# Performance work log

Hardware: AMD Instinct MI355X
Metric: run time of the kernel (lower is better)

## Reference

```python
import jax, jax.numpy as jnp
import numpy as np

N = 262144          # ray samples
L = 16              # grid levels
T = 2 ** 19         # hash table entries per level
F = 2               # features per entry
NMIN, NMAX = 16, 2048
SB = 1.0            # scene_bound
DW, CW = 64, 64     # density / color MLP widths

_PRIMES = jnp.array([1, 2654435761, 805459861], dtype=jnp.uint32)
_OFFS = jnp.asarray(np.stack(np.meshgrid([0, 1], [0, 1], [0, 1], indexing='ij'), -1).reshape(8, 3), dtype=jnp.uint32)  # 8 cube corners


def _scalings():
    g = np.exp((np.log(NMAX) - np.log(NMIN)) / (L - 1))
    return jnp.asarray(np.floor(NMIN * g ** np.arange(L)), dtype=jnp.float32)  # (L,)


def hash_encode(pos01, table):
    # pos01: (N,3) in [0,1]; table: (L*T, F)
    scaled = pos01[:, None, :] * _scalings()[None, :, None]        # (N,L,3)
    floor = jnp.floor(scaled)
    frac = scaled - floor                                          # (N,L,3)
    corners = floor.astype(jnp.uint32)[:, :, None, :] + _OFFS[None, None]  # (N,L,8,3)
    h = corners * _PRIMES                                          # uint32 wraparound hashing
    idx = (h[..., 0] ^ h[..., 1] ^ h[..., 2]) % jnp.uint32(T)      # (N,L,8)
    idx = idx.astype(jnp.int32) + (jnp.arange(L, dtype=jnp.int32) * T)[None, :, None]
    feats = table[idx]                                             # (N,L,8,F) gather
    sel = _OFFS.astype(bool)[None, None]                           # (1,1,8,3)
    w = jnp.prod(jnp.where(sel, frac[:, :, None, :], 1.0 - frac[:, :, None, :]), axis=-1)  # (N,L,8)
    out = jnp.einsum('nlcf,nlc->nlf', feats, w)                    # trilinear interp
    return out.reshape(out.shape[0], L * F)                        # (N, 32)


def sh_encode(d):
    # 4th-order real spherical harmonics, 16 components (instant-ngp convention)
    x, y, z = d[..., 0], d[..., 1], d[..., 2]
    xx, yy, zz = x * x, y * y, z * z
    xy, yz, xz = x * y, y * z, x * z
    return jnp.stack([
        jnp.full_like(x, 0.28209479177387814),
        -0.48860251190291987 * y,
        0.48860251190291987 * z,
        -0.48860251190291987 * x,
        1.0925484305920792 * xy,
        -1.0925484305920792 * yz,
        0.94617469575755997 * zz - 0.31539156525252005,
        -1.0925484305920792 * xz,
        0.54627421529603959 * (xx - yy),
        0.59004358992664352 * y * (-3.0 * xx + yy),
        2.8906114426405538 * xy * z,
        0.45704579946446572 * y * (1.0 - 5.0 * zz),
        0.3731763325901154 * z * (5.0 * zz - 3.0),
        0.45704579946446572 * x * (1.0 - 5.0 * zz),
        1.445305721320277 * z * (xx - yy),
        0.59004358992664352 * x * (xx - 3.0 * yy),
    ], axis=-1)  # (N,16)


def setup_inputs() -> dict:
    key = jax.random.key(0)
    ks = jax.random.split(key, 10)
    position = jax.random.uniform(ks[0], (N, 3), jnp.float32, -SB, SB)
    d = jax.random.normal(ks[1], (N, 3), jnp.float32)
    direction = d / jnp.linalg.norm(d, axis=-1, keepdims=True)
    hash_table = jax.random.uniform(ks[2], (L * T, F), jnp.float32, -1e-4, 1e-4)
    def dense(k, fin, fout, std):
        return (jax.random.normal(k, (fin, fout), jnp.float32) * std,
                jnp.zeros((fout,), jnp.float32))
    w1, b1 = dense(ks[3], L * F, DW, 0.01)      # normal() init in source
    w2, b2 = dense(ks[4], DW, 16, 0.01)
    w3, b3 = dense(ks[5], 16 + 16, CW, 0.01)
    w4, b4 = dense(ks[6], CW, CW, 0.01)
    w5, b5 = dense(ks[7], CW, 3, 0.1)           # default lecun-ish scale
    return dict(position=position, direction=direction, hash_table=hash_table,
                w1=w1, b1=b1, w2=w2, b2=b2, w3=w3, b3=b3, w4=w4, b4=b4, w5=w5, b5=b5)


def reference(position, direction, hash_table, w1, b1, w2, b2, w3, b3, w4, b4, w5, b5):
    p = (position + SB) / (2.0 * SB)                 # -> [0,1]
    enc = hash_encode(p, hash_table)                 # (N,32)
    h = jax.nn.relu(enc @ w1 + b1)                   # density MLP
    h = h @ w2 + b2                                  # (N,16)
    density = jnp.exp(h[:, 0:1])                     # exponential_density_activation
    sh = sh_encode(direction)                        # (N,16)
    c = jnp.concatenate([h, sh], axis=-1)            # (N,32)
    c = jax.nn.relu(c @ w3 + b3)
    c = jax.nn.relu(c @ w4 + b4)
    c = c @ w5 + b5
    color = jax.nn.sigmoid(c)                        # high_dynamic_range=False
    return jnp.concatenate([density, color], axis=-1)  # (N,4) drgbs
```

## Files before the change

kernel.cpp:

```cpp
#include <hip/hip_runtime.h>
#include <cmath>

namespace {
constexpr int kN = 262144;
constexpr int kL = 16;
constexpr int kT = 1 << 19;
constexpr unsigned kTMask = kT - 1;

typedef __attribute__((ext_vector_type(8))) short short8;
typedef __attribute__((ext_vector_type(4))) float f32x4;
typedef __attribute__((ext_vector_type(4))) unsigned short ushort4v;

struct Scales { float s[kL]; };

__device__ __forceinline__ unsigned short f2bf(float f) {
    unsigned u = __builtin_bit_cast(unsigned, f);
    return (unsigned short)((u + 0x7FFFu + ((u >> 16) & 1u)) >> 16);
}

__global__ __launch_bounds__(256) void prep_w(
    const float* __restrict__ w1, const float* __restrict__ w2,
    const float* __restrict__ w3, const float* __restrict__ w4,
    const float* __restrict__ w5, unsigned short* __restrict__ out)
{
    const int i = blockIdx.x * 256 + threadIdx.x;
    const int f = i >> 9;
    const int l = (i >> 3) & 63;
    const int e = i & 7;
    const int cl = l & 15;
    const int kg = l >> 4;
    float v = 0.0f;
    if (f < 4) {
        v = w1[(kg * 8 + e) * 64 + f * 16 + cl];
    } else if (f < 6) {
        const int q = f - 4;
        v = w2[(q * 32 + kg * 8 + e) * 16 + cl];
    } else if (f < 10) {
        v = w3[(kg * 8 + e) * 64 + (f - 6) * 16 + cl];
    } else if (f < 18) {
        const int g = f - 10, q = g >> 2, nt = g & 3;
        v = w4[(q * 32 + kg * 8 + e) * 64 + nt * 16 + cl];
    } else {
        const int q = f - 18;
        v = (cl < 3) ? w5[(q * 32 + kg * 8 + e) * 3 + cl] : 0.0f;
    }
    out[i] = f2bf(v);
}

__global__ __launch_bounds__(256) void ngp_encode(
    const float* __restrict__ pos,
    const float2* __restrict__ table,
    unsigned* __restrict__ enc,
    Scales sc)
{
    const int bid = blockIdx.x;
    const int l = bid >> 10;
    const int n = ((bid & 1023) << 8) | threadIdx.x;

    const float s = sc.s[l];
    const float2* __restrict__ tl = table + (size_t)l * kT;

    const float px = (pos[n * 3 + 0] + 1.0f) * 0.5f;
    const float py = (pos[n * 3 + 1] + 1.0f) * 0.5f;
    const float pz = (pos[n * 3 + 2] + 1.0f) * 0.5f;
    const float sx = px * s, sy = py * s, sz = pz * s;
    const float fx = floorf(sx), fy = floorf(sy), fz = floorf(sz);
    const float rx = sx - fx, ry = sy - fy, rz = sz - fz;
    const unsigned cx = (unsigned)fx, cy = (unsigned)fy, cz = (unsigned)fz;

    const unsigned hy0 = cy * 2654435761u, hy1 = (cy + 1u) * 2654435761u;
    const unsigned hz0 = cz * 805459861u,  hz1 = (cz + 1u) * 805459861u;

    float4 pr[4];
    float2 ex[4];
    unsigned idx0v[4], hyzv[4];

    #pragma unroll
    for (int j = 0; j < 4; ++j) {
        const unsigned hyz = ((j >> 1) ? hy1 : hy0) ^ ((j & 1) ? hz1 : hz0);
        hyzv[j] = hyz;
        const unsigned idx0 = (cx ^ hyz) & kTMask;
        idx0v[j] = idx0;
        pr[j] = *reinterpret_cast<const float4*>(tl + (idx0 & ~1u));
    }

    if (cx & 1u) {
        const unsigned cx1 = cx + 1u;
        #pragma unroll
        for (int j = 0; j < 4; ++j)
            ex[j] = tl[(cx1 ^ hyzv[j]) & kTMask];
    }

    const bool odd = (cx & 1u) != 0u;
    const float wx0 = 1.0f - rx, wx1 = rx;
    float f0 = 0.f, f1 = 0.f;
    #pragma unroll
    for (int j = 0; j < 4; ++j) {
        const float wyz = ((j >> 1) ? ry : 1.0f - ry) *
                          ((j & 1) ? rz : 1.0f - rz);
        const bool hi = (idx0v[j] & 1u) != 0u;
        const float c0x = hi ? pr[j].z : pr[j].x;
        const float c0y = hi ? pr[j].w : pr[j].y;
        const float c1x = odd ? ex[j].x : (hi ? pr[j].x : pr[j].z);
        const float c1y = odd ? ex[j].y : (hi ? pr[j].y : pr[j].w);
        f0 = fmaf(c0x, wx0 * wyz, f0);
        f1 = fmaf(c0y, wx0 * wyz, f1);
        f0 = fmaf(c1x, wx1 * wyz, f0);
        f1 = fmaf(c1y, wx1 * wyz, f1);
    }
    enc[(size_t)l * kN + n] = (unsigned)f2bf(f0) | ((unsigned)f2bf(f1) << 16);
}

__global__ __launch_bounds__(256) void ngp_mlp_mfma(
    const unsigned* __restrict__ enc,
    const unsigned short* __restrict__ wbf,
    const float* __restrict__ dir,
    const float* __restrict__ b1, const float* __restrict__ b2,
    const float* __restrict__ b3, const float* __restrict__ b4,
    const float* __restrict__ b5,
    float* __restrict__ out)
{
    __shared__ unsigned short sA[4][4096];
    __shared__ unsigned short sB[4][2048];

    const int tid = threadIdx.x;
    const int wid = tid >> 6;
    const int l   = tid & 63;
    const int cl  = l & 15;
    const int kg  = l >> 4;
    unsigned short* __restrict__ A_ = sA[wid];
    unsigned short* __restrict__ B_ = sB[wid];
    const int gbase = blockIdx.x * 256 + wid * 64;

    {
        const int s = gbase + l;
        const float x = dir[s * 3 + 0], y = dir[s * 3 + 1], z = dir[s * 3 + 2];
        const float xx = x * x, yy = y * y, zz = z * z;
        const float xy = x * y, yz = y * z, xz = x * z;
        float sh[16];
        sh[0] = 0.28209479177387814f;
        sh[1] = -0.48860251190291987f * y;
        sh[2] = 0.48860251190291987f * z;
        sh[3] = -0.48860251190291987f * x;
        sh[4] = 1.0925484305920792f * xy;
        sh[5] = -1.0925484305920792f * yz;
        sh[6] = 0.94617469575755997f * zz - 0.31539156525252005f;
        sh[7] = -1.0925484305920792f * xz;
        sh[8] = 0.54627421529603959f * (xx - yy);
        sh[9] = 0.59004358992664352f * y * (-3.0f * xx + yy);
        sh[10] = 2.8906114426405538f * xy * z;
        sh[11] = 0.45704579946446572f * y * (1.0f - 5.0f * zz);
        sh[12] = 0.3731763325901154f * z * (5.0f * zz - 3.0f);
        sh[13] = 0.45704579946446572f * x * (1.0f - 5.0f * zz);
        sh[14] = 1.445305721320277f * z * (xx - yy);
        sh[15] = 0.59004358992664352f * x * (xx - 3.0f * yy);
        #pragma unroll
        for (int j = 0; j < 16; ++j)
            B_[(l >> 4) * 512 + (16 + j) * 16 + (l & 15)] = f2bf(sh[j]);
    }

    short8 A1[4];
    #pragma unroll
    for (int m = 0; m < 4; ++m) {
        #pragma unroll
        for (int j = 0; j < 4; ++j) {
            const unsigned v = enc[(size_t)(kg * 4 + j) * kN + (gbase + m * 16 + cl)];
            A1[m][2 * j]     = (short)(v & 0xFFFFu);
            A1[m][2 * j + 1] = (short)(v >> 16);
        }
    }
    {
        short8 B1[4];
        #pragma unroll
        for (int nt = 0; nt < 4; ++nt)
            B1[nt] = *reinterpret_cast<const short8*>(&wbf[(size_t)(nt) * 512 + l * 8]);

        f32x4 acc[4][4];
        #pragma unroll
        for (int nt = 0; nt < 4; ++nt) {
            const float bv = b1[nt * 16 + cl];
            #pragma unroll
            for (int m = 0; m < 4; ++m) {
                acc[m][nt][0] = bv; acc[m][nt][1] = bv; acc[m][nt][2] = bv; acc[m][nt][3] = bv;
            }
        }
        #pragma unroll
        for (int m = 0; m < 4; ++m)
            #pragma unroll
            for (int nt = 0; nt < 4; ++nt)
                acc[m][nt] = __builtin_amdgcn_mfma_f32_16x16x32_bf16(A1[m], B1[nt], acc[m][nt], 0, 0, 0);

        #pragma unroll
        for (int m = 0; m < 4; ++m) {
            #pragma unroll
            for (int nt = 0; nt < 4; ++nt) {
                ushort4v pk;
                #pragma unroll
                for (int r = 0; r < 4; ++r) pk[r] = f2bf(fmaxf(acc[m][nt][r], 0.0f));
                *reinterpret_cast<ushort4v*>(&A_[m * 1024 + (nt * 16 + cl) * 16 + kg * 4]) = pk;
            }
        }
    }

    {
        short8 A2[4][2];
        #pragma unroll
        for (int m = 0; m < 4; ++m)
            #pragma unroll
            for (int q = 0; q < 2; ++q)
                #pragma unroll
                for (int e = 0; e < 8; ++e)
                    A2[m][q][e] = (short)A_[m * 1024 + (q * 32 + kg * 8 + e) * 16 + cl];

        short8 B2[2];
        #pragma unroll
        for (int q = 0; q < 2; ++q)
            B2[q] = *reinterpret_cast<const short8*>(&wbf[(size_t)(4 + q) * 512 + l * 8]);

        f32x4 acc[4];
        const float bv = b2[cl];
        #pragma unroll
        for (int m = 0; m < 4; ++m) { acc[m][0] = bv; acc[m][1] = bv; acc[m][2] = bv; acc[m][3] = bv; }
        #pragma unroll
        for (int m = 0; m < 4; ++m)
            #pragma unroll
            for (int q = 0; q < 2; ++q)
                acc[m] = __builtin_amdgcn_mfma_f32_16x16x32_bf16(A2[m][q], B2[q], acc[m], 0, 0, 0);

        #pragma unroll
        for (int m = 0; m < 4; ++m) {
            if (cl == 0) {
                #pragma unroll
                for (int r = 0; r < 4; ++r)
                    out[(size_t)(gbase + m * 16 + kg * 4 + r) * 4 + 0] = expf(acc[m][r]);
            }
            ushort4v pk;
            #pragma unroll
            for (int r = 0; r < 4; ++r) pk[r] = f2bf(acc[m][r]);
            *reinterpret_cast<ushort4v*>(&B_[m * 512 + cl * 16 + kg * 4]) = pk;
        }
    }

    {
        short8 A3[4];
        #pragma unroll
        for (int m = 0; m < 4; ++m)
            #pragma unroll
            for (int e = 0; e < 8; ++e)
                A3[m][e] = (short)B_[m * 512 + (kg * 8 + e) * 16 + cl];

        short8 B3[4];
        #pragma unroll
        for (int nt = 0; nt < 4; ++nt)
            B3[nt] = *reinterpret_cast<const short8*>(&wbf[(size_t)(6 + nt) * 512 + l * 8]);

        f32x4 acc[4][4];
        #pragma unroll
        for (int nt = 0; nt < 4; ++nt) {
            const float bv = b3[nt * 16 + cl];
            #pragma unroll
            for (int m = 0; m < 4; ++m) {
                acc[m][nt][0] = bv; acc[m][nt][1] = bv; acc[m][nt][2] = bv; acc[m][nt][3] = bv;
            }
        }
        #pragma unroll
        for (int m = 0; m < 4; ++m)
            #pragma unroll
            for (int nt = 0; nt < 4; ++nt)
                acc[m][nt] = __builtin_amdgcn_mfma_f32_16x16x32_bf16(A3[m], B3[nt], acc[m][nt], 0, 0, 0);

        #pragma unroll
        for (int m = 0; m < 4; ++m) {
            #pragma unroll
            for (int nt = 0; nt < 4; ++nt) {
                ushort4v pk;
                #pragma unroll
                for (int r = 0; r < 4; ++r) pk[r] = f2bf(fmaxf(acc[m][nt][r], 0.0f));
                *reinterpret_cast<ushort4v*>(&A_[m * 1024 + (nt * 16 + cl) * 16 + kg * 4]) = pk;
            }
        }
    }

    {
        short8 A4[4][2];
        #pragma unroll
        for (int m = 0; m < 4; ++m)
            #pragma unroll
            for (int q = 0; q < 2; ++q)
                #pragma unroll
                for (int e = 0; e < 8; ++e)
                    A4[m][q][e] = (short)A_[m * 1024 + (q * 32 + kg * 8 + e) * 16 + cl];

        short8 B4[2][4];
        #pragma unroll
        for (int q = 0; q < 2; ++q)
            #pragma unroll
            for (int nt = 0; nt < 4; ++nt)
                B4[q][nt] = *reinterpret_cast<const short8*>(&wbf[(size_t)(10 + q * 4 + nt) * 512 + l * 8]);

        f32x4 acc[4][4];
        #pragma unroll
        for (int nt = 0; nt < 4; ++nt) {
            const float bv = b4[nt * 16 + cl];
            #pragma unroll
            for (int m = 0; m < 4; ++m) {
                acc[m][nt][0] = bv; acc[m][nt][1] = bv; acc[m][nt][2] = bv; acc[m][nt][3] = bv;
            }
        }
        #pragma unroll
        for (int m = 0; m < 4; ++m)
            #pragma unroll
            for (int nt = 0; nt < 4; ++nt)
                #pragma unroll
                for (int q = 0; q < 2; ++q)
                    acc[m][nt] = __builtin_amdgcn_mfma_f32_16x16x32_bf16(A4[m][q], B4[q][nt], acc[m][nt], 0, 0, 0);

        #pragma unroll
        for (int m = 0; m < 4; ++m) {
            #pragma unroll
            for (int nt = 0; nt < 4; ++nt) {
                ushort4v pk;
                #pragma unroll
                for (int r = 0; r < 4; ++r) pk[r] = f2bf(fmaxf(acc[m][nt][r], 0.0f));
                *reinterpret_cast<ushort4v*>(&A_[m * 1024 + (nt * 16 + cl) * 16 + kg * 4]) = pk;
            }
        }
    }

    {
        short8 A5[4][2];
        #pragma unroll
        for (int m = 0; m < 4; ++m)
            #pragma unroll
            for (int q = 0; q < 2; ++q)
                #pragma unroll
                for (int e = 0; e < 8; ++e)
                    A5[m][q][e] = (short)A_[m * 1024 + (q * 32 + kg * 8 + e) * 16 + cl];

        short8 B5[2];
        #pragma unroll
        for (int q = 0; q < 2; ++q)
            B5[q] = *reinterpret_cast<const short8*>(&wbf[(size_t)(18 + q) * 512 + l * 8]);

        f32x4 acc[4];
        const float bv = (cl < 3) ? b5[cl] : 0.0f;
        #pragma unroll
        for (int m = 0; m < 4; ++m) { acc[m][0] = bv; acc[m][1] = bv; acc[m][2] = bv; acc[m][3] = bv; }
        #pragma unroll
        for (int m = 0; m < 4; ++m)
            #pragma unroll
            for (int q = 0; q < 2; ++q)
                acc[m] = __builtin_amdgcn_mfma_f32_16x16x32_bf16(A5[m][q], B5[q], acc[m], 0, 0, 0);

        if (cl < 3) {
            #pragma unroll
            for (int m = 0; m < 4; ++m)
                #pragma unroll
                for (int r = 0; r < 4; ++r)
                    out[(size_t)(gbase + m * 16 + kg * 4 + r) * 4 + 1 + cl] =
                        1.0f / (1.0f + expf(-acc[m][r]));
        }
    }
}

}

extern "C" void kernel_launch(void* const* d_in, const int* in_sizes, int n_in,
                              void* d_out, int out_size, void* d_ws, size_t ws_size,
                              hipStream_t stream) {
    (void)in_sizes; (void)n_in; (void)out_size; (void)ws_size;

    Scales sc;
    const double g = exp((log(2048.0) - log(16.0)) / 15.0);
    for (int l = 0; l < kL; ++l) sc.s[l] = (float)floor(16.0 * pow(g, (double)l));

    const float*  pos   = (const float*)d_in[0];
    const float*  dir   = (const float*)d_in[1];
    const float2* table = (const float2*)d_in[2];
    const float *w1 = (const float*)d_in[3],  *b1 = (const float*)d_in[4];
    const float *w2 = (const float*)d_in[5],  *b2 = (const float*)d_in[6];
    const float *w3 = (const float*)d_in[7],  *b3 = (const float*)d_in[8];
    const float *w4 = (const float*)d_in[9],  *b4 = (const float*)d_in[10];
    const float *w5 = (const float*)d_in[11], *b5 = (const float*)d_in[12];
    float* out = (float*)d_out;

    unsigned short* wbf = (unsigned short*)d_ws;
    unsigned* enc = (unsigned*)((char*)d_ws + 32768);

    prep_w<<<40, 256, 0, stream>>>(w1, w2, w3, w4, w5, wbf);
    ngp_encode<<<kL * 1024, 256, 0, stream>>>(pos, table, enc, sc);
    ngp_mlp_mfma<<<kN / 256, 256, 0, stream>>>(enc, wbf, dir,
        b1, b2, b3, b4, b5, out);
}
```

Measured before the change: 147.4 us.

## Spatially bucket-sort ray samples before hash encoding to improve gather locality

Adds histogram, scan and scatter kernels that reorder samples by a coarse 16^3 spatial cell, so the encode kernel processes nearby points together and hash-table gathers for coarse levels share cache lines. The MLP reads sorted directions and writes outputs back through a sorted-to-original index map. This costs extra launches, contended atomics, a single-block scan, and scattered output writes.

```diff
diff --git a/kernel.cpp b/kernel.cpp
--- a/kernel.cpp
+++ b/kernel.cpp
@@ -6,6 +6,7 @@
 constexpr int kL = 16;
 constexpr int kT = 1 << 19;
 constexpr unsigned kTMask = kT - 1;
+constexpr int kB = 4096;
 
 typedef __attribute__((ext_vector_type(8))) short short8;
 typedef __attribute__((ext_vector_type(4))) float f32x4;
@@ -47,8 +48,69 @@
     out[i] = f2bf(v);
 }
 
+__global__ __launch_bounds__(256) void bucket_hist(
+    const float* __restrict__ pos,
+    unsigned short* __restrict__ key,
+    unsigned* __restrict__ hist)
+{
+    const int n = blockIdx.x * 256 + threadIdx.x;
+    const float px = (pos[n * 3 + 0] + 1.0f) * 0.5f;
+    const float py = (pos[n * 3 + 1] + 1.0f) * 0.5f;
+    const float pz = (pos[n * 3 + 2] + 1.0f) * 0.5f;
+    const int cx = min(15, (int)(px * 16.0f));
+    const int cy = min(15, (int)(py * 16.0f));
+    const int cz = min(15, (int)(pz * 16.0f));
+    const int k = (cx << 8) | (cy << 4) | cz;
+    key[n] = (unsigned short)k;
+    atomicAdd(&hist[k], 1u);
+}
+
+__global__ __launch_bounds__(1024) void bucket_scan(
+    const unsigned* __restrict__ hist,
+    unsigned* __restrict__ cursor)
+{
+    __shared__ unsigned s[1024];
+    const int t = threadIdx.x;
+    const unsigned v0 = hist[4 * t], v1 = hist[4 * t + 1];
+    const unsigned v2 = hist[4 * t + 2], v3 = hist[4 * t + 3];
+    const unsigned a0 = v0, a1 = a0 + v1, a2 = a1 + v2, a3 = a2 + v3;
+    s[t] = a3;
+    __syncthreads();
+    for (int off = 1; off < 1024; off <<= 1) {
+        unsigned x = 0;
+        if (t >= off) x = s[t - off];
+        __syncthreads();
+        if (t >= off) s[t] += x;
+        __syncthreads();
+    }
+    const unsigned base = (t > 0) ? s[t - 1] : 0u;
+    cursor[4 * t]     = base;
+    cursor[4 * t + 1] = base + a0;
+    cursor[4 * t + 2] = base + a1;
+    cursor[4 * t + 3] = base + a2;
+}
+
+__global__ __launch_bounds__(256) void bucket_scatter(
+    const float* __restrict__ pos, const float* __restrict__ dir,
+    const unsigned short* __restrict__ key,
+    unsigned* __restrict__ cursor,
+    float* __restrict__ spos, float* __restrict__ sdir,
+    unsigned* __restrict__ s2o)
+{
+    const int n = blockIdx.x * 256 + threadIdx.x;
+    const unsigned k = key[n];
+    const unsigned i = atomicAdd(&cursor[k], 1u);
+    s2o[i] = (unsigned)n;
+    spos[i * 3 + 0] = pos[n * 3 + 0];
+    spos[i * 3 + 1] = pos[n * 3 + 1];
+    spos[i * 3 + 2] = pos[n * 3 + 2];
+    sdir[i * 3 + 0] = dir[n * 3 + 0];
+    sdir[i * 3 + 1] = dir[n * 3 + 1];
+    sdir[i * 3 + 2] = dir[n * 3 + 2];
+}
+
 __global__ __launch_bounds__(256) void ngp_encode(
-    const float* __restrict__ pos,
+    const float* __restrict__ spos,
     const float2* __restrict__ table,
     unsigned* __restrict__ enc,
     Scales sc)
@@ -60,9 +122,9 @@
     const float s = sc.s[l];
     const float2* __restrict__ tl = table + (size_t)l * kT;
 
-    const float px = (pos[n * 3 + 0] + 1.0f) * 0.5f;
-    const float py = (pos[n * 3 + 1] + 1.0f) * 0.5f;
-    const float pz = (pos[n * 3 + 2] + 1.0f) * 0.5f;
+    const float px = (spos[n * 3 + 0] + 1.0f) * 0.5f;
+    const float py = (spos[n * 3 + 1] + 1.0f) * 0.5f;
+    const float pz = (spos[n * 3 + 2] + 1.0f) * 0.5f;
     const float sx = px * s, sy = py * s, sz = pz * s;
     const float fx = floorf(sx), fy = floorf(sy), fz = floorf(sz);
     const float rx = sx - fx, ry = sy - fy, rz = sz - fz;
@@ -114,7 +176,8 @@
 __global__ __launch_bounds__(256) void ngp_mlp_mfma(
     const unsigned* __restrict__ enc,
     const unsigned short* __restrict__ wbf,
-    const float* __restrict__ dir,
+    const float* __restrict__ sdir,
+    const unsigned* __restrict__ s2o,
     const float* __restrict__ b1, const float* __restrict__ b2,
     const float* __restrict__ b3, const float* __restrict__ b4,
     const float* __restrict__ b5,
@@ -134,7 +197,7 @@
 
     {
         const int s = gbase + l;
-        const float x = dir[s * 3 + 0], y = dir[s * 3 + 1], z = dir[s * 3 + 2];
+        const float x = sdir[s * 3 + 0], y = sdir[s * 3 + 1], z = sdir[s * 3 + 2];
         const float xx = x * x, yy = y * y, zz = z * z;
         const float xy = x * y, yz = y * z, xz = x * z;
         float sh[16];
@@ -232,7 +295,7 @@
             if (cl == 0) {
                 #pragma unroll
                 for (int r = 0; r < 4; ++r)
-                    out[(size_t)(gbase + m * 16 + kg * 4 + r) * 4 + 0] = expf(acc[m][r]);
+                    out[(size_t)s2o[gbase + m * 16 + kg * 4 + r] * 4 + 0] = expf(acc[m][r]);
             }
             ushort4v pk;
             #pragma unroll
@@ -357,7 +420,7 @@
             for (int m = 0; m < 4; ++m)
                 #pragma unroll
                 for (int r = 0; r < 4; ++r)
-                    out[(size_t)(gbase + m * 16 + kg * 4 + r) * 4 + 1 + cl] =
+                    out[(size_t)s2o[gbase + m * 16 + kg * 4 + r] * 4 + 1 + cl] =
                         1.0f / (1.0f + expf(-acc[m][r]));
         }
     }
@@ -384,11 +447,22 @@
     const float *w5 = (const float*)d_in[11], *b5 = (const float*)d_in[12];
     float* out = (float*)d_out;
 
-    unsigned short* wbf = (unsigned short*)d_ws;
-    unsigned* enc = (unsigned*)((char*)d_ws + 32768);
-
+    char* ws = (char*)d_ws;
+    unsigned short* wbf   = (unsigned short*)(ws);
+    unsigned*       hist  = (unsigned*)(ws + 65536);
+    unsigned*       cursor= (unsigned*)(ws + 81920);
+    unsigned short* key   = (unsigned short*)(ws + 98304);
+    unsigned*       s2o   = (unsigned*)(ws + 622592);
+    float*          spos  = (float*)(ws + 1671168);
+    float*          sdir  = (float*)(ws + 4816896);
+    unsigned*       enc   = (unsigned*)(ws + 7962624);
+
+    hipMemsetAsync(hist, 0, kB * sizeof(unsigned), stream);
     prep_w<<<40, 256, 0, stream>>>(w1, w2, w3, w4, w5, wbf);
-    ngp_encode<<<kL * 1024, 256, 0, stream>>>(pos, table, enc, sc);
-    ngp_mlp_mfma<<<kN / 256, 256, 0, stream>>>(enc, wbf, dir,
+    bucket_hist<<<kN / 256, 256, 0, stream>>>(pos, key, hist);
+    bucket_scan<<<1, 1024, 0, stream>>>(hist, cursor);
+    bucket_scatter<<<kN / 256, 256, 0, stream>>>(pos, dir, key, cursor, spos, sdir, s2o);
+    ngp_encode<<<kL * 1024, 256, 0, stream>>>(spos, table, enc, sc);
+    ngp_mlp_mfma<<<kN / 256, 256, 0, stream>>>(enc, wbf, sdir, s2o,
         b1, b2, b3, b4, b5, out);
 }
```

Result: slower. 167.9 us (+13.9%).
